# Optimization experiments

Hardware: AMD Instinct MI355X
Metric: run time of the kernel (lower is better)

Reference implementation:

```python
import jax, jax.numpy as jnp
import numpy as np

B, S, D, H = 8, 2048, 512, 512


def setup_inputs() -> dict:
    key = jax.random.key(0)
    ks = jax.random.split(key, 5)
    scale = 0.05
    x = jax.random.normal(ks[0], (B, S, D), dtype=jnp.float32)
    Wq = jax.random.normal(ks[1], (D, H), dtype=jnp.float32) * scale
    Wk = jax.random.normal(ks[2], (D, H), dtype=jnp.float32) * scale
    Wv = jax.random.normal(ks[3], (D, H), dtype=jnp.float32) * scale
    Wo = jax.random.normal(ks[4], (H, D), dtype=jnp.float32) * scale
    bq = jnp.zeros((H,), dtype=jnp.float32)
    bk = jnp.zeros((H,), dtype=jnp.float32)
    bv = jnp.zeros((H,), dtype=jnp.float32)
    bo = jnp.zeros((D,), dtype=jnp.float32)
    return {"x": x, "Wq": Wq, "bq": bq, "Wk": Wk, "bk": bk,
            "Wv": Wv, "bv": bv, "Wo": Wo, "bo": bo}


def reference(x, Wq, bq, Wk, bk, Wv, bv, Wo, bo):
    # x: [B, S, D]
    q = jnp.einsum('bsd,dh->bsh', x, Wq) + bq  # [B,S,H]
    k = jnp.einsum('bsd,dh->bsh', x, Wk) + bk
    v = jnp.einsum('bsd,dh->bsh', x, Wv) + bv
    scores = jnp.einsum('bqh,bkh->bqk', q, k) / jnp.sqrt(jnp.float32(H))  # [B,S,S]
    weights = jax.nn.softmax(scores, axis=-1)
    context = jnp.einsum('bqk,bkh->bqh', weights, v)  # [B,S,H]
    out = jnp.einsum('bsh,hd->bsd', context, Wo) + bo  # [B,S,D]
    return out + x
```

## Files before the change

kernel.cpp:

```cpp
#include <hip/hip_runtime.h>
#include <stdint.h>


typedef __attribute__((ext_vector_type(4))) float f32x4;
typedef __attribute__((ext_vector_type(8))) short short8;
typedef __attribute__((ext_vector_type(4))) unsigned short ushort4v;
typedef __attribute__((ext_vector_type(8))) unsigned short ushort8v;
typedef unsigned short bf16_t;

#define AS1 __attribute__((address_space(1)))
#define AS3 __attribute__((address_space(3)))

static __device__ __forceinline__ unsigned short f2bf(float f) {
  unsigned int u = __float_as_uint(f);
  u += 0x7fffu + ((u >> 16) & 1u);
  return (unsigned short)(u >> 16);
}
static __device__ __forceinline__ float bf2f(unsigned short h) {
  return __uint_as_float(((unsigned int)h) << 16);
}

__global__ __launch_bounds__(256) void ws_sentinel(float* out) {
  out[threadIdx.x] = 1e30f;
}

__global__ __launch_bounds__(256) void cast_f32_bf16(
    const float* __restrict__ in, bf16_t* __restrict__ out, int n4) {
  int i = blockIdx.x * 256 + threadIdx.x;
  if (i >= n4) return;
  float4 v = ((const float4*)in)[i];
  ushort4v o = { f2bf(v.x), f2bf(v.y), f2bf(v.z), f2bf(v.w) };
  ((ushort4v*)out)[i] = o;
}

__global__ __launch_bounds__(256) void cast_transpose_w(
    const float* __restrict__ Wq, const float* __restrict__ Wk,
    const float* __restrict__ Wv, const float* __restrict__ Wo,
    bf16_t* __restrict__ WqkvT, bf16_t* __restrict__ WoT) {
  __shared__ float tile[32][33];
  int z = blockIdx.z;
  const float* in = (z == 0) ? Wq : (z == 1) ? Wk : (z == 2) ? Wv : Wo;
  bf16_t* out = (z < 3) ? WqkvT + z * 512 * 512 : WoT;
  int bx = blockIdx.x * 32;
  int by = blockIdx.y * 32;
  int tx = threadIdx.x & 31;
  int ty = threadIdx.x >> 5;
#pragma unroll
  for (int k = 0; k < 4; ++k)
    tile[ty + k * 8][tx] = in[(by + ty + k * 8) * 512 + bx + tx];
  __syncthreads();
#pragma unroll
  for (int k = 0; k < 4; ++k)
    out[(bx + ty + k * 8) * 512 + by + tx] = f2bf(tile[tx][ty + k * 8]);
}

__global__ __launch_bounds__(256) void concat_bias(
    const float* __restrict__ b0, const float* __restrict__ b1,
    const float* __restrict__ b2, float* __restrict__ out) {
  int i = blockIdx.x * 256 + threadIdx.x;
  const float* src = (i < 512) ? b0 : (i < 1024) ? b1 : b2;
  out[i] = src[i & 511];
}

template <typename OT>
__global__ __launch_bounds__(256, 2) void gemm_bt(
    const bf16_t* __restrict__ A, int lda, long sA,
    const bf16_t* __restrict__ BT, int ldb, long sB,
    const float* __restrict__ bias, const float* __restrict__ resid,
    bf16_t* __restrict__ vt_out,
    OT* __restrict__ Cout, int ldc, long sC, int M, int N, int K, float scale) {
  __shared__ __align__(16) bf16_t As[128 * 64];
  __shared__ __align__(16) bf16_t Bs[128 * 64];
  const int z = blockIdx.z;
  const bf16_t* Ab = A + (long)z * sA;
  const bf16_t* Bb = BT + (long)z * sB;
  const int tile_m = blockIdx.x * 128;
  const int tile_n = blockIdx.y * 128;
  const int t = threadIdx.x;
  const int lane = t & 63;
  const int wave = t >> 6;
  const int wm = (wave >> 1) * 64;
  const int wn = (wave & 1) * 64;

  f32x4 acc[4][4];
#pragma unroll
  for (int i = 0; i < 4; ++i)
#pragma unroll
    for (int j = 0; j < 4; ++j) acc[i][j] = f32x4{0.f, 0.f, 0.f, 0.f};

  const bf16_t* gA[4];
  const bf16_t* gB[4];
  int ldsoff[4];
#pragma unroll
  for (int i = 0; i < 4; ++i) {
    int o16 = i * 256 + t;
    int row = o16 >> 3;
    int slot = (o16 & 7) ^ (row & 7);
    gA[i] = Ab + (long)(tile_m + row) * lda + slot * 8;
    gB[i] = Bb + (long)(tile_n + row) * ldb + slot * 8;
    ldsoff[i] = o16 * 8;
  }

  const int nk = K >> 6;
  for (int kt = 0; kt < nk; ++kt) {
#pragma unroll
    for (int i = 0; i < 4; ++i) {
      __builtin_amdgcn_global_load_lds((const AS1 unsigned int*)(gA[i]),
                                       (AS3 unsigned int*)(&As[ldsoff[i]]),
                                       16, 0, 0);
      __builtin_amdgcn_global_load_lds((const AS1 unsigned int*)(gB[i]),
                                       (AS3 unsigned int*)(&Bs[ldsoff[i]]),
                                       16, 0, 0);
      gA[i] += 64;
      gB[i] += 64;
    }
    __syncthreads();
#pragma unroll
    for (int ks = 0; ks < 2; ++ks) {
      short8 af[4], bfr[4];
#pragma unroll
      for (int i = 0; i < 4; ++i) {
        int ra = wm + i * 16 + (lane & 15);
        int oa = ra * 128 + ((ks * 64 + (lane >> 4) * 16) ^ ((ra & 7) << 4));
        af[i] = *(const short8*)((const char*)As + oa);
        int rb = wn + i * 16 + (lane & 15);
        int ob = rb * 128 + ((ks * 64 + (lane >> 4) * 16) ^ ((rb & 7) << 4));
        bfr[i] = *(const short8*)((const char*)Bs + ob);
      }
#pragma unroll
      for (int i = 0; i < 4; ++i)
#pragma unroll
        for (int j = 0; j < 4; ++j)
          acc[i][j] = __builtin_amdgcn_mfma_f32_16x16x32_bf16(
              af[i], bfr[j], acc[i][j], 0, 0, 0);
    }
    __syncthreads();
  }

  OT* Cz = Cout + (long)z * sC;
#pragma unroll
  for (int i = 0; i < 4; ++i) {
    int crow0 = tile_m + wm + i * 16 + ((lane >> 4) << 2);
#pragma unroll
    for (int j = 0; j < 4; ++j) {
      int ccol = tile_n + wn + j * 16 + (lane & 15);
      float bv = bias ? bias[ccol] : 0.f;
      if (vt_out && ccol >= 1024) {
        int c = ccol - 1024;
#pragma unroll
        for (int r = 0; r < 4; ++r) {
          int rr = crow0 + r;
          float val = acc[i][j][r] * scale + bv;
          vt_out[((long)(rr >> 11) << 20) + ((long)c << 11) + (rr & 2047)] =
              f2bf(val);
        }
      } else {
#pragma unroll
        for (int r = 0; r < 4; ++r) {
          long idx = (long)(crow0 + r) * ldc + ccol;
          float val = acc[i][j][r] * scale + bv;
          if (resid) val += resid[idx];
          if constexpr (sizeof(OT) == 2)
            Cz[idx] = (OT)f2bf(val);
          else
            Cz[idx] = (OT)val;
        }
      }
    }
  }
}

__global__ __launch_bounds__(256, 4) void softmax_rows_bf16(
    bf16_t* __restrict__ S) {
  long row = blockIdx.x;
  bf16_t* srow = S + row * 2048;
  int t = threadIdx.x;
  ushort8v v = *(ushort8v*)(srow + t * 8);
  float e[8];
#pragma unroll
  for (int k = 0; k < 8; ++k) e[k] = bf2f(v[k]);
  float m = e[0];
#pragma unroll
  for (int k = 1; k < 8; ++k) m = fmaxf(m, e[k]);
#pragma unroll
  for (int off = 32; off; off >>= 1) m = fmaxf(m, __shfl_xor(m, off, 64));
  __shared__ float red[8];
  if ((t & 63) == 0) red[t >> 6] = m;
  __syncthreads();
  m = fmaxf(fmaxf(red[0], red[1]), fmaxf(red[2], red[3]));
  float s = 0.f;
#pragma unroll
  for (int k = 0; k < 8; ++k) {
    e[k] = __expf(e[k] - m);
    s += e[k];
  }
#pragma unroll
  for (int off = 32; off; off >>= 1) s += __shfl_xor(s, off, 64);
  if ((t & 63) == 0) red[4 + (t >> 6)] = s;
  __syncthreads();
  s = (red[4] + red[5]) + (red[6] + red[7]);
  float inv = 1.0f / s;
  ushort8v o;
#pragma unroll
  for (int k = 0; k < 8; ++k) o[k] = f2bf(e[k] * inv);
  *(ushort8v*)(srow + t * 8) = o;
}

extern "C" void kernel_launch(void* const* d_in, const int* in_sizes, int n_in,
                              void* d_out, int out_size, void* d_ws,
                              size_t ws_size, hipStream_t stream) {
  const float* x  = (const float*)d_in[0];
  const float* Wq = (const float*)d_in[1];
  const float* bq = (const float*)d_in[2];
  const float* Wk = (const float*)d_in[3];
  const float* bk = (const float*)d_in[4];
  const float* Wv = (const float*)d_in[5];
  const float* bv = (const float*)d_in[6];
  const float* Wo = (const float*)d_in[7];
  const float* bo = (const float*)d_in[8];
  float* out = (float*)d_out;

  const int S = 2048, D = 512;
  const long MS = 16384;
  const long MB = 1024 * 1024;

  const size_t need = 147 * MB;
  if (ws_size < need) {
    ws_sentinel<<<1, 256, 0, stream>>>(out);
    return;
  }
  char* w = (char*)d_ws;
  bf16_t* xb    = (bf16_t*)(w);
  bf16_t* ctx   = (bf16_t*)(w);
  bf16_t* QKV   = (bf16_t*)(w + 16 * MB);
  bf16_t* VT    = (bf16_t*)(w + 64 * MB);
  bf16_t* Sc    = (bf16_t*)(w + 80 * MB);
  bf16_t* WqkvT = (bf16_t*)(w + 144 * MB);
  bf16_t* WoT   = WqkvT + 1536 * 512;
  float*  bqkv  = (float*)(WoT + 512 * 512);

  cast_f32_bf16<<<dim3(8192), 256, 0, stream>>>(x, xb, (int)(MS * D / 4));
  cast_transpose_w<<<dim3(16, 16, 4), 256, 0, stream>>>(Wq, Wk, Wv, Wo,
                                                        WqkvT, WoT);
  concat_bias<<<dim3(6), 256, 0, stream>>>(bq, bk, bv, bqkv);

  gemm_bt<bf16_t><<<dim3(128, 12), 256, 0, stream>>>(
      xb, 512, 0, WqkvT, 512, 0, bqkv, nullptr, VT,
      QKV, 1536, 0, 16384, 1536, 512, 1.0f);

  const float rsq = 0.04419417382415922f;
  gemm_bt<bf16_t><<<dim3(16, 16, 8), 256, 0, stream>>>(
      QKV, 1536, (long)S * 1536, QKV + 512, 1536, (long)S * 1536,
      nullptr, nullptr, nullptr, Sc, 2048, (long)S * S, 2048, 2048, 512, rsq);

  softmax_rows_bf16<<<dim3(16384), 256, 0, stream>>>(Sc);

  gemm_bt<bf16_t><<<dim3(16, 4, 8), 256, 0, stream>>>(
      Sc, 2048, (long)S * 2048, VT, 2048, (long)512 * S,
      nullptr, nullptr, nullptr, ctx, 512, (long)S * 512, 2048, 512, 2048,
      1.0f);

  gemm_bt<float><<<dim3(128, 4), 256, 0, stream>>>(
      ctx, 512, 0, WoT, 512, 0, bo, x, nullptr, out, 512, 0,
      16384, 512, 512, 1.0f);
}
```

Before: 290.3 us.

## Add 256-row tiled 512-thread GEMM for attention score and context matmuls

Introduces a new templated GEMM kernel with 256xBN block tiles, 8 waves, double-buffered LDS filled by direct global-to-LDS loads and XOR-swizzled layout. It replaces the generic gemm_bt for the QK^T and PV batched matmuls. Larger tiles raise operand reuse and cut global traffic per FLOP. The cost is larger LDS use and more accumulator registers, which can limit occupancy, and the PV grid of 256 blocks may not fill every CU.

```diff
diff --git a/kernel.cpp b/kernel.cpp
--- a/kernel.cpp
+++ b/kernel.cpp
@@ -170,6 +170,123 @@
   }
 }
 
+template <int BN>
+__global__ __launch_bounds__(512, 2) void gemm256(
+    const bf16_t* __restrict__ A, int lda, long sA,
+    const bf16_t* __restrict__ BT, int ldb, long sB,
+    bf16_t* __restrict__ Cout, int ldc, long sC, int K, float scale) {
+  constexpr int JF = BN / 64;
+  constexpr int BCH = BN * 8 / 512;
+  __shared__ __align__(16) bf16_t As[2][256 * 64];
+  __shared__ __align__(16) bf16_t Bs[2][BN * 64];
+  const int z = blockIdx.z;
+  const bf16_t* Ab = A + (long)z * sA;
+  const bf16_t* Bb = BT + (long)z * sB;
+  const int tile_m = blockIdx.x * 256;
+  const int tile_n = blockIdx.y * BN;
+  const int t = threadIdx.x;
+  const int lane = t & 63;
+  const int wave = t >> 6;
+  const int wm = (wave >> 2) * 128;
+  const int wn = (wave & 3) * (BN / 4);
+
+  f32x4 acc[8][JF];
+#pragma unroll
+  for (int i = 0; i < 8; ++i)
+#pragma unroll
+    for (int j = 0; j < JF; ++j) acc[i][j] = f32x4{0.f, 0.f, 0.f, 0.f};
+
+  const bf16_t* gA[4];
+  int ldsA[4];
+#pragma unroll
+  for (int k = 0; k < 4; ++k) {
+    int c = k * 512 + t;
+    int row = c >> 3;
+    int slot = (c & 7) ^ (row & 7);
+    gA[k] = Ab + (long)(tile_m + row) * lda + slot * 8;
+    ldsA[k] = c * 8;
+  }
+  const bf16_t* gB[BCH];
+  int ldsB[BCH];
+#pragma unroll
+  for (int k = 0; k < BCH; ++k) {
+    int c = k * 512 + t;
+    int row = c >> 3;
+    int slot = (c & 7) ^ (row & 7);
+    gB[k] = Bb + (long)(tile_n + row) * ldb + slot * 8;
+    ldsB[k] = c * 8;
+  }
+
+  const int nk = K >> 6;
+  int buf = 0;
+#pragma unroll
+  for (int k = 0; k < 4; ++k)
+    __builtin_amdgcn_global_load_lds((const AS1 unsigned int*)(gA[k]),
+                                     (AS3 unsigned int*)(&As[0][ldsA[k]]),
+                                     16, 0, 0);
+#pragma unroll
+  for (int k = 0; k < BCH; ++k)
+    __builtin_amdgcn_global_load_lds((const AS1 unsigned int*)(gB[k]),
+                                     (AS3 unsigned int*)(&Bs[0][ldsB[k]]),
+                                     16, 0, 0);
+  __syncthreads();
+
+  for (int kt = 0; kt < nk; ++kt) {
+    if (kt + 1 < nk) {
+      long koff = (long)(kt + 1) * 64;
+#pragma unroll
+      for (int k = 0; k < 4; ++k)
+        __builtin_amdgcn_global_load_lds(
+            (const AS1 unsigned int*)(gA[k] + koff),
+            (AS3 unsigned int*)(&As[buf ^ 1][ldsA[k]]), 16, 0, 0);
+#pragma unroll
+      for (int k = 0; k < BCH; ++k)
+        __builtin_amdgcn_global_load_lds(
+            (const AS1 unsigned int*)(gB[k] + koff),
+            (AS3 unsigned int*)(&Bs[buf ^ 1][ldsB[k]]), 16, 0, 0);
+    }
+    const char* Ap = (const char*)As[buf];
+    const char* Bp = (const char*)Bs[buf];
+#pragma unroll
+    for (int ks = 0; ks < 2; ++ks) {
+      short8 af[8], bfr[JF];
+#pragma unroll
+      for (int i = 0; i < 8; ++i) {
+        int ra = wm + i * 16 + (lane & 15);
+        int oa = ra * 128 + ((ks * 64 + (lane >> 4) * 16) ^ ((ra & 7) << 4));
+        af[i] = *(const short8*)(Ap + oa);
+      }
+#pragma unroll
+      for (int j = 0; j < JF; ++j) {
+        int rb = wn + j * 16 + (lane & 15);
+        int ob = rb * 128 + ((ks * 64 + (lane >> 4) * 16) ^ ((rb & 7) << 4));
+        bfr[j] = *(const short8*)(Bp + ob);
+      }
+#pragma unroll
+      for (int i = 0; i < 8; ++i)
+#pragma unroll
+        for (int j = 0; j < JF; ++j)
+          acc[i][j] = __builtin_amdgcn_mfma_f32_16x16x32_bf16(
+              af[i], bfr[j], acc[i][j], 0, 0, 0);
+    }
+    __syncthreads();
+    buf ^= 1;
+  }
+
+  bf16_t* Cz = Cout + (long)z * sC;
+#pragma unroll
+  for (int i = 0; i < 8; ++i) {
+    int crow0 = tile_m + wm + i * 16 + ((lane >> 4) << 2);
+#pragma unroll
+    for (int j = 0; j < JF; ++j) {
+      int ccol = tile_n + wn + j * 16 + (lane & 15);
+#pragma unroll
+      for (int r = 0; r < 4; ++r)
+        Cz[(long)(crow0 + r) * ldc + ccol] = f2bf(acc[i][j][r] * scale);
+    }
+  }
+}
+
 __global__ __launch_bounds__(256, 4) void softmax_rows_bf16(
     bf16_t* __restrict__ S) {
   long row = blockIdx.x;
@@ -249,16 +366,15 @@
       QKV, 1536, 0, 16384, 1536, 512, 1.0f);
 
   const float rsq = 0.04419417382415922f;
-  gemm_bt<bf16_t><<<dim3(16, 16, 8), 256, 0, stream>>>(
+  gemm256<256><<<dim3(8, 8, 8), 512, 0, stream>>>(
       QKV, 1536, (long)S * 1536, QKV + 512, 1536, (long)S * 1536,
-      nullptr, nullptr, nullptr, Sc, 2048, (long)S * S, 2048, 2048, 512, rsq);
+      Sc, 2048, (long)S * S, 512, rsq);
 
   softmax_rows_bf16<<<dim3(16384), 256, 0, stream>>>(Sc);
 
-  gemm_bt<bf16_t><<<dim3(16, 4, 8), 256, 0, stream>>>(
+  gemm256<128><<<dim3(8, 4, 8), 512, 0, stream>>>(
       Sc, 2048, (long)S * 2048, VT, 2048, (long)512 * S,
-      nullptr, nullptr, nullptr, ctx, 512, (long)S * 512, 2048, 512, 2048,
-      1.0f);
+      ctx, 512, (long)S * 512, 2048, 1.0f);
 
   gemm_bt<float><<<dim3(128, 4), 256, 0, stream>>>(
       ctx, 512, 0, WoT, 512, 0, bo, x, nullptr, out, 512, 0,
```

Result: faster. 273.7 us (-5.7%).
